# Kernel optimization log

Measured on AMD Instinct MI355X. Metric: run time of the kernel, lower is better.

Reference implementation:

```python
import math
import jax, jax.numpy as jnp
import numpy as np

B, S, E, H = 4, 2048, 1024, 16
HD = E // H  # 64


def setup_inputs() -> dict:
    key = jax.random.key(0)
    ks = jax.random.split(key, 7)
    scale = 1.0 / math.sqrt(E)
    return {
        "x": jax.random.normal(ks[0], (B, S, E), dtype=jnp.float32),
        "Wq": jax.random.normal(ks[1], (H, HD, E), dtype=jnp.float32) * scale,
        "bq": jax.random.normal(ks[2], (H, HD), dtype=jnp.float32) * 0.01,
        "Wk": jax.random.normal(ks[3], (H, HD, E), dtype=jnp.float32) * scale,
        "bk": jax.random.normal(ks[4], (H, HD), dtype=jnp.float32) * 0.01,
        "Wv": jax.random.normal(ks[5], (H, HD, E), dtype=jnp.float32) * scale,
        "bv": jax.random.normal(ks[6], (H, HD), dtype=jnp.float32) * 0.01,
    }


def reference(x, Wq, bq, Wk, bk, Wv, bv):
    b, s, e = x.shape
    h, hd, _ = Wq.shape
    inv_scale = 1.0 / math.sqrt(hd)
    # per-head linear projections (torch Linear: x @ W^T + b), batched over heads
    q = jnp.einsum("bse,hde->bshd", x, Wq) + bq  # [B,S,H,HD]
    k = jnp.einsum("bse,hde->bshd", x, Wk) + bk
    v = jnp.einsum("bse,hde->bshd", x, Wv) + bv
    # causal mask: -inf above diagonal (added before scaling, as in source;
    # -inf * inv_scale is still -inf so math is identical)
    mask = jnp.triu(jnp.full((s, s), -jnp.inf, dtype=x.dtype), k=1)
    scores = (jnp.einsum("bqhd,bkhd->bhqk", q, k) + mask) * inv_scale  # [B,H,S,S]
    attn = jax.nn.softmax(scores, axis=-1)
    out = jnp.einsum("bhqk,bkhd->bqhd", attn, v)  # [B,S,H,HD]
    # concat over heads in head order == reshape with head-major last dims
    return out.reshape(b, s, h * hd)
```

## Files before the change

### kernel.cpp

```cpp
#include <hip/hip_runtime.h>


typedef __bf16 bf16x8 __attribute__((ext_vector_type(8)));
typedef __bf16 bf16x4 __attribute__((ext_vector_type(4)));
typedef float f32x4 __attribute__((ext_vector_type(4)));
typedef unsigned short us8 __attribute__((ext_vector_type(8)));
typedef unsigned short us4 __attribute__((ext_vector_type(4)));

#define Bb 4
#define Ss 2048
#define Ee 1024
#define Hh 16
#define HD 64

#if __has_builtin(__builtin_amdgcn_exp2f)
#define EXP2(x) __builtin_amdgcn_exp2f(x)
#else
#define EXP2(x) exp2f(x)
#endif

__device__ __forceinline__ unsigned short f2bf(float f) {
  union { float f; unsigned u; } v; v.f = f;
  unsigned u = v.u;
  u += 0x7fffu + ((u >> 16) & 1u);
  return (unsigned short)(u >> 16);
}

__device__ __forceinline__ void gl_lds16(const void* g, void* l) {
  __builtin_amdgcn_global_load_lds((const __attribute__((address_space(1))) void*)g,
                                   (__attribute__((address_space(3))) void*)l, 16, 0, 0);
}

__global__ __launch_bounds__(256) void cvt_all(const float* __restrict__ x,
                                               const float* __restrict__ wq,
                                               const float* __restrict__ wk,
                                               const float* __restrict__ wv,
                                               unsigned short* __restrict__ xb,
                                               unsigned short* __restrict__ wb) {
  int i = blockIdx.x * 256 + threadIdx.x;
  const float* src; unsigned short* dst; int idx;
  if (i < 2097152)      { src = x;  dst = xb;                idx = i; }
  else if (i < 2359296) { src = wq; dst = wb;                idx = i - 2097152; }
  else if (i < 2621440) { src = wk; dst = wb + 1048576;      idx = i - 2359296; }
  else                  { src = wv; dst = wb + 2 * 1048576;  idx = i - 2621440; }
  float4 f = ((const float4*)src)[idx];
  us4 o = { f2bf(f.x), f2bf(f.y), f2bf(f.z), f2bf(f.w) };
  ((us4*)dst)[idx] = o;
}

__global__ __launch_bounds__(256) void qkv_gemm(const unsigned short* __restrict__ xb,
                                                const unsigned short* __restrict__ wb_all,
                                                const float* __restrict__ bq,
                                                const float* __restrict__ bk,
                                                const float* __restrict__ bv,
                                                unsigned short* __restrict__ qkv) {
  const int z = blockIdx.z;
  const unsigned short* wb = wb_all + (size_t)z * (Ee * Ee);
  const float* bias = (z == 0) ? bq : (z == 1) ? bk : bv;
  unsigned short* outb = qkv + (size_t)z * (Bb * Ss * Ee);
  const float osc = (z == 0) ? 0.180336880f : 1.0f;

  __shared__ unsigned short SMEM[16384];
  unsigned short* As = SMEM;
  unsigned short* Bs = SMEM + 8192;

  const int t = threadIdx.x;
  const int wave = t >> 6, lane = t & 63, quad = lane >> 4, ln = lane & 15;
  const int wm = wave & 1, wn = wave >> 1;
  const int m0 = blockIdx.x * 128, n0 = blockIdx.y * 128;

  const int srow = t >> 2;
  const int scol = (t & 3) * 8;

  f32x4 acc[4][4] = {};

  const unsigned short* ga = xb + (size_t)(m0 + srow) * Ee + scol;
  const unsigned short* gb = wb + (size_t)(n0 + srow) * Ee + scol;
  unsigned short* la = &As[t * 8];
  unsigned short* lb = &Bs[t * 8];

  for (int k0 = 0; k0 < Ee; k0 += 64) {
    __syncthreads();
    gl_lds16(ga + k0,                la);
    gl_lds16(ga + k0 + 64 * Ee,      la + 64 * 32);
    gl_lds16(gb + k0,                lb);
    gl_lds16(gb + k0 + 64 * Ee,      lb + 64 * 32);
    gl_lds16(ga + k0 + 32,           la + 4096);
    gl_lds16(ga + k0 + 32 + 64 * Ee, la + 4096 + 64 * 32);
    gl_lds16(gb + k0 + 32,           lb + 4096);
    gl_lds16(gb + k0 + 32 + 64 * Ee, lb + 4096 + 64 * 32);
    __syncthreads();
#pragma unroll
    for (int p = 0; p < 2; ++p) {
      bf16x8 af[4], bfr[4];
#pragma unroll
      for (int i = 0; i < 4; ++i)
        af[i] = *(const bf16x8*)&As[p * 4096 + (wm * 64 + i * 16 + ln) * 32 + quad * 8];
#pragma unroll
      for (int j = 0; j < 4; ++j)
        bfr[j] = *(const bf16x8*)&Bs[p * 4096 + (wn * 64 + j * 16 + ln) * 32 + quad * 8];
#pragma unroll
      for (int i = 0; i < 4; ++i)
#pragma unroll
        for (int j = 0; j < 4; ++j)
          acc[i][j] = __builtin_amdgcn_mfma_f32_16x16x32_bf16(af[i], bfr[j], acc[i][j], 0, 0, 0);
    }
  }

  float biasj[4];
#pragma unroll
  for (int j = 0; j < 4; ++j) biasj[j] = bias[n0 + wn * 64 + j * 16 + ln];

  if (z != 2) {
#pragma unroll
    for (int i = 0; i < 4; ++i)
#pragma unroll
      for (int j = 0; j < 4; ++j)
#pragma unroll
        for (int r = 0; r < 4; ++r) {
          int m = m0 + wm * 64 + i * 16 + quad * 4 + r;
          int n = n0 + wn * 64 + j * 16 + ln;
          int b_ = m >> 11, s = m & 2047;
          int h = n >> 6, d = n & 63;
          outb[(((size_t)b_ * Hh + h) * Ss + s) * HD + d] = f2bf((acc[i][j][r] + biasj[j]) * osc);
        }
  } else {
    for (int half = 0; half < 2; ++half) {
      __syncthreads();
      if (wm == half) {
#pragma unroll
        for (int i = 0; i < 4; ++i)
#pragma unroll
          for (int j = 0; j < 4; ++j)
#pragma unroll
            for (int r = 0; r < 4; ++r) {
              int mr = i * 16 + quad * 4 + r;
              int nc = wn * 64 + j * 16 + ln;
              SMEM[nc * 72 + mr] = f2bf(acc[i][j][r] + biasj[j]);
            }
      }
      __syncthreads();
      int nr = t >> 1;
      int n = n0 + nr;
      int h = n >> 6, d = n & 63;
      int mbase = m0 + half * 64 + (t & 1) * 32;
      int b_ = mbase >> 11;
#pragma unroll
      for (int q = 0; q < 4; ++q) {
        int s = (mbase & 2047) + q * 8;
        us8 vdat = *(const us8*)&SMEM[nr * 72 + (t & 1) * 32 + q * 8];
        *(us8*)&outb[(((size_t)b_ * Hh + h) * HD + d) * Ss + s] = vdat;
      }
    }
  }
}

__global__ __launch_bounds__(256) void flash_attn(const unsigned short* __restrict__ qkv,
                                                  float* __restrict__ out) {
  const int id = blockIdx.x;
  const int bh = id & 63;
  const int p = id >> 6;
  const int b_ = bh >> 4, h = bh & 15;

  const unsigned short* qb  = qkv + (size_t)bh * (Ss * HD);
  const unsigned short* kb  = qkv + (size_t)(64 + bh) * (Ss * HD);
  const unsigned short* vtb = qkv + (size_t)(128 + bh) * (Ss * HD);

  __shared__ __bf16 Ks[4096];
  __shared__ __bf16 Vt[4096];
  __shared__ __bf16 Ps[4][2][16][72];

  const int t = threadIdx.x;
  const int wave = t >> 6, lane = t & 63, quad = lane >> 4, ln = lane & 15;

  const int r0 = t >> 3;
  const int c0 = ((t & 7) ^ (r0 & 7)) * 8;
  const int koff0 = r0 * HD + c0;
  const int koff1 = koff0 + 32 * HD;
  const int voff0 = r0 * Ss + c0;
  const int voff1 = voff0 + 32 * Ss;
  __bf16* Kl0 = &Ks[t * 8];  __bf16* Kl1 = &Ks[2048 + t * 8];
  __bf16* Vl0 = &Vt[t * 8];  __bf16* Vl1 = &Vt[2048 + t * 8];

  int kslot[4][2];
#pragma unroll
  for (int g = 0; g < 4; ++g)
#pragma unroll
    for (int ks = 0; ks < 2; ++ks)
      kslot[g][ks] = ((g * 16 + ln) * 8 + ((ks * 4 + quad) ^ (ln & 7))) * 8;

  bf16x8 onef;
#pragma unroll
  for (int j = 0; j < 8; ++j) onef[j] = (__bf16)1.0f;

  const int qtps[2] = { 15 - p, p };

  for (int ph = 0; ph < 2; ++ph) {
    const int qtp = qtps[ph];
    const int q0 = qtp * 128;

    bf16x8 qf[2][2];
#pragma unroll
    for (int u = 0; u < 2; ++u)
#pragma unroll
      for (int ks = 0; ks < 2; ++ks)
        qf[u][ks] = *(const bf16x8*)(qb + (size_t)(q0 + u * 64 + wave * 16 + ln) * HD +
                                     ks * 32 + quad * 8);

    f32x4 o[2][4] = {};
    f32x4 l4[2] = {};
    const int ktmax = 2 * qtp + 1;

    for (int kt = 0; kt <= ktmax; ++kt) {
      const unsigned short* kbt = kb + kt * (64 * HD);
      const unsigned short* vbt = vtb + kt * 64;
      __syncthreads();
      gl_lds16(kbt + koff0, Kl0);
      gl_lds16(kbt + koff1, Kl1);
      gl_lds16(vbt + voff0, Vl0);
      gl_lds16(vbt + voff1, Vl1);
      __syncthreads();

#pragma unroll
      for (int u = 0; u < 2; ++u) {
        if (u == 0 && kt == ktmax) continue;
        const int qrow = q0 + u * 64 + wave * 16 + ln;

        f32x4 s_acc[4] = {};
#pragma unroll
        for (int g = 0; g < 4; ++g)
#pragma unroll
          for (int ks = 0; ks < 2; ++ks) {
            bf16x8 kf = *(const bf16x8*)&Ks[kslot[g][ks]];
            s_acc[g] = __builtin_amdgcn_mfma_f32_16x16x32_bf16(kf, qf[u][ks], s_acc[g], 0, 0, 0);
          }

        if (kt == 2 * qtp + u) {
          const int k0 = kt * 64;
#pragma unroll
          for (int g = 0; g < 4; ++g)
#pragma unroll
            for (int r = 0; r < 4; ++r) {
              int kcol = k0 + g * 16 + quad * 4 + r;
              if (kcol > qrow) s_acc[g][r] = -__builtin_inff();
            }
        }

#pragma unroll
        for (int g = 0; g < 4; ++g) {
          bf16x4 pk = { (__bf16)EXP2(s_acc[g][0]), (__bf16)EXP2(s_acc[g][1]),
                        (__bf16)EXP2(s_acc[g][2]), (__bf16)EXP2(s_acc[g][3]) };
          *(bf16x4*)&Ps[wave][u][ln][g * 16 + quad * 4] = pk;
        }
        bf16x8 pf[2];
#pragma unroll
        for (int ks = 0; ks < 2; ++ks)
          pf[ks] = *(const bf16x8*)&Ps[wave][u][ln][ks * 32 + quad * 8];

        l4[u] = __builtin_amdgcn_mfma_f32_16x16x32_bf16(pf[0], onef, l4[u], 0, 0, 0);
        l4[u] = __builtin_amdgcn_mfma_f32_16x16x32_bf16(pf[1], onef, l4[u], 0, 0, 0);

#pragma unroll
        for (int g = 0; g < 4; ++g)
#pragma unroll
          for (int ks = 0; ks < 2; ++ks) {
            bf16x8 vf = *(const bf16x8*)&Vt[kslot[g][ks]];
            o[u][g] = __builtin_amdgcn_mfma_f32_16x16x32_bf16(pf[ks], vf, o[u][g], 0, 0, 0);
          }
      }
    }

#pragma unroll
    for (int u = 0; u < 2; ++u) {
      float linv[4];
#pragma unroll
      for (int r = 0; r < 4; ++r) linv[r] = 1.0f / l4[u][r];
#pragma unroll
      for (int g = 0; g < 4; ++g)
#pragma unroll
        for (int r = 0; r < 4; ++r) {
          int orow = q0 + u * 64 + wave * 16 + quad * 4 + r;
          out[((size_t)b_ * Ss + orow) * Ee + h * HD + g * 16 + ln] = o[u][g][r] * linv[r];
        }
    }
    __syncthreads();
  }
}

extern "C" void kernel_launch(void* const* d_in, const int* in_sizes, int n_in,
                              void* d_out, int out_size, void* d_ws, size_t ws_size,
                              hipStream_t stream) {
  const float* x  = (const float*)d_in[0];
  const float* Wq = (const float*)d_in[1];
  const float* bq = (const float*)d_in[2];
  const float* Wk = (const float*)d_in[3];
  const float* bk = (const float*)d_in[4];
  const float* Wv = (const float*)d_in[5];
  const float* bv = (const float*)d_in[6];
  float* out = (float*)d_out;

  unsigned short* ws  = (unsigned short*)d_ws;
  unsigned short* xb  = ws;
  unsigned short* wb  = ws + 8388608;
  unsigned short* qkv = ws + 8388608 + 3 * 1048576;

  cvt_all<<<11264, 256, 0, stream>>>(x, Wq, Wk, Wv, xb, wb);
  qkv_gemm<<<dim3(64, 8, 3), 256, 0, stream>>>(xb, wb, bq, bk, bv, qkv);
  flash_attn<<<512, 256, 0, stream>>>(qkv, out);
}
```

Measured before the change: 219.9 us.

## Rewrite QKV GEMM with 256x256 tiles, double-buffered LDS and swizzled layout

The QKV projection GEMM moves from 128x128 tiles with 256 threads to 256x256 tiles with 512 threads. It double-buffers LDS across K steps, interleaving the next tile's global-to-LDS loads with MFMA quadrants, gated by explicit vmcnt waits, barriers and setprio. LDS is XOR-swizzled to avoid bank conflicts. The aim is to raise data reuse per block and hide global load latency. The cost is a 128 KB LDS footprint, only 384 blocks, and fragile hand-written synchronisation.

```diff
diff --git a/kernel.cpp b/kernel.cpp
--- a/kernel.cpp
+++ b/kernel.cpp
@@ -48,108 +48,235 @@
   ((us4*)dst)[idx] = o;
 }
 
-__global__ __launch_bounds__(256) void qkv_gemm(const unsigned short* __restrict__ xb,
-                                                const unsigned short* __restrict__ wb_all,
-                                                const float* __restrict__ bq,
-                                                const float* __restrict__ bk,
-                                                const float* __restrict__ bv,
-                                                unsigned short* __restrict__ qkv) {
+__global__ __launch_bounds__(512, 2) void qkv_gemm(const unsigned short* __restrict__ xb,
+                                                   const unsigned short* __restrict__ wb_all,
+                                                   const float* __restrict__ bq,
+                                                   const float* __restrict__ bk,
+                                                   const float* __restrict__ bv,
+                                                   unsigned short* __restrict__ qkv) {
   const int z = blockIdx.z;
   const unsigned short* wb = wb_all + (size_t)z * (Ee * Ee);
   const float* bias = (z == 0) ? bq : (z == 1) ? bk : bv;
   unsigned short* outb = qkv + (size_t)z * (Bb * Ss * Ee);
   const float osc = (z == 0) ? 0.180336880f : 1.0f;
 
-  __shared__ unsigned short SMEM[16384];
-  unsigned short* As = SMEM;
-  unsigned short* Bs = SMEM + 8192;
+  __shared__ unsigned short SMEM[65536];
 
   const int t = threadIdx.x;
   const int wave = t >> 6, lane = t & 63, quad = lane >> 4, ln = lane & 15;
-  const int wm = wave & 1, wn = wave >> 1;
-  const int m0 = blockIdx.x * 128, n0 = blockIdx.y * 128;
-
-  const int srow = t >> 2;
-  const int scol = (t & 3) * 8;
-
-  f32x4 acc[4][4] = {};
-
-  const unsigned short* ga = xb + (size_t)(m0 + srow) * Ee + scol;
-  const unsigned short* gb = wb + (size_t)(n0 + srow) * Ee + scol;
-  unsigned short* la = &As[t * 8];
-  unsigned short* lb = &Bs[t * 8];
-
-  for (int k0 = 0; k0 < Ee; k0 += 64) {
-    __syncthreads();
-    gl_lds16(ga + k0,                la);
-    gl_lds16(ga + k0 + 64 * Ee,      la + 64 * 32);
-    gl_lds16(gb + k0,                lb);
-    gl_lds16(gb + k0 + 64 * Ee,      lb + 64 * 32);
-    gl_lds16(ga + k0 + 32,           la + 4096);
-    gl_lds16(ga + k0 + 32 + 64 * Ee, la + 4096 + 64 * 32);
-    gl_lds16(gb + k0 + 32,           lb + 4096);
-    gl_lds16(gb + k0 + 32 + 64 * Ee, lb + 4096 + 64 * 32);
-    __syncthreads();
-#pragma unroll
-    for (int p = 0; p < 2; ++p) {
-      bf16x8 af[4], bfr[4];
-#pragma unroll
-      for (int i = 0; i < 4; ++i)
-        af[i] = *(const bf16x8*)&As[p * 4096 + (wm * 64 + i * 16 + ln) * 32 + quad * 8];
-#pragma unroll
-      for (int j = 0; j < 4; ++j)
-        bfr[j] = *(const bf16x8*)&Bs[p * 4096 + (wn * 64 + j * 16 + ln) * 32 + quad * 8];
-#pragma unroll
-      for (int i = 0; i < 4; ++i)
-#pragma unroll
-        for (int j = 0; j < 4; ++j)
-          acc[i][j] = __builtin_amdgcn_mfma_f32_16x16x32_bf16(af[i], bfr[j], acc[i][j], 0, 0, 0);
-    }
+  const int wr = wave >> 2, wc = wave & 3;
+  const int m0 = blockIdx.x * 256, n0 = blockIdx.y * 256;
+
+  const int r8 = t >> 3;
+  const int cs = ((t & 7) ^ (r8 & 7)) * 8;
+  const int t8 = t * 8;
+  const unsigned short* gA0 = xb + (size_t)(m0 + r8) * Ee + cs;
+  const unsigned short* gA1 = gA0 + 128 * Ee;
+  const unsigned short* gB0 = wb + (size_t)(n0 + r8) * Ee + cs;
+  const unsigned short* gB1 = gB0 + 128 * Ee;
+
+  int aoff0[4][2], boff0[2][2];
+#pragma unroll
+  for (int i = 0; i < 4; ++i)
+#pragma unroll
+    for (int kk = 0; kk < 2; ++kk)
+      aoff0[i][kk] = (wr * 64 + i * 16 + ln) * 64 + (((kk * 4 + quad) ^ (ln & 7)) * 8);
+#pragma unroll
+  for (int j = 0; j < 2; ++j)
+#pragma unroll
+    for (int kk = 0; kk < 2; ++kk)
+      boff0[j][kk] = 16384 + (wc * 32 + j * 16 + ln) * 64 + (((kk * 4 + quad) ^ (ln & 7)) * 8);
+
+  f32x4 acc[2][2][4][2] = {};
+
+  gl_lds16(gA0,           &SMEM[t8]);
+  gl_lds16(gA0 + 64 * Ee, &SMEM[t8 + 4096]);
+  gl_lds16(gB0,           &SMEM[16384 + t8]);
+  gl_lds16(gB0 + 64 * Ee, &SMEM[16384 + t8 + 4096]);
+  gl_lds16(gB1,           &SMEM[24576 + t8]);
+  gl_lds16(gB1 + 64 * Ee, &SMEM[24576 + t8 + 4096]);
+  gl_lds16(gA1,           &SMEM[8192 + t8]);
+  gl_lds16(gA1 + 64 * Ee, &SMEM[8192 + t8 + 4096]);
+
+#pragma unroll 1
+  for (int kt = 0; kt < 15; ++kt) {
+    const int cbuf = (kt & 1) << 15;
+    const int sbuf = cbuf ^ 32768;
+    const int co = (kt + 1) * 64;
+
+    bf16x8 af[4][2], bf0[2][2], bf1[2][2];
+
+    asm volatile("s_waitcnt vmcnt(4)" ::: "memory");
+    asm volatile("s_barrier" ::: "memory");
+#pragma unroll
+    for (int i = 0; i < 4; ++i)
+#pragma unroll
+      for (int kk = 0; kk < 2; ++kk)
+        af[i][kk] = *(const bf16x8*)&SMEM[cbuf + aoff0[i][kk]];
+#pragma unroll
+    for (int j = 0; j < 2; ++j)
+#pragma unroll
+      for (int kk = 0; kk < 2; ++kk)
+        bf0[j][kk] = *(const bf16x8*)&SMEM[cbuf + boff0[j][kk]];
+    gl_lds16(gA0 + co,           &SMEM[sbuf + t8]);
+    gl_lds16(gA0 + co + 64 * Ee, &SMEM[sbuf + t8 + 4096]);
+    asm volatile("s_barrier" ::: "memory");
+    __builtin_amdgcn_s_setprio(1);
+#pragma unroll
+    for (int i = 0; i < 4; ++i)
+#pragma unroll
+      for (int j = 0; j < 2; ++j)
+#pragma unroll
+        for (int kk = 0; kk < 2; ++kk)
+          acc[0][0][i][j] = __builtin_amdgcn_mfma_f32_16x16x32_bf16(af[i][kk], bf0[j][kk], acc[0][0][i][j], 0, 0, 0);
+    __builtin_amdgcn_s_setprio(0);
+
+    asm volatile("s_waitcnt vmcnt(4)" ::: "memory");
+    asm volatile("s_barrier" ::: "memory");
+#pragma unroll
+    for (int j = 0; j < 2; ++j)
+#pragma unroll
+      for (int kk = 0; kk < 2; ++kk)
+        bf1[j][kk] = *(const bf16x8*)&SMEM[cbuf + boff0[j][kk] + 8192];
+    gl_lds16(gB0 + co,           &SMEM[sbuf + 16384 + t8]);
+    gl_lds16(gB0 + co + 64 * Ee, &SMEM[sbuf + 16384 + t8 + 4096]);
+    asm volatile("s_barrier" ::: "memory");
+    __builtin_amdgcn_s_setprio(1);
+#pragma unroll
+    for (int i = 0; i < 4; ++i)
+#pragma unroll
+      for (int j = 0; j < 2; ++j)
+#pragma unroll
+        for (int kk = 0; kk < 2; ++kk)
+          acc[0][1][i][j] = __builtin_amdgcn_mfma_f32_16x16x32_bf16(af[i][kk], bf1[j][kk], acc[0][1][i][j], 0, 0, 0);
+    __builtin_amdgcn_s_setprio(0);
+
+    asm volatile("s_waitcnt vmcnt(4)" ::: "memory");
+    asm volatile("s_barrier" ::: "memory");
+#pragma unroll
+    for (int i = 0; i < 4; ++i)
+#pragma unroll
+      for (int kk = 0; kk < 2; ++kk)
+        af[i][kk] = *(const bf16x8*)&SMEM[cbuf + aoff0[i][kk] + 8192];
+    gl_lds16(gB1 + co,           &SMEM[sbuf + 24576 + t8]);
+    gl_lds16(gB1 + co + 64 * Ee, &SMEM[sbuf + 24576 + t8 + 4096]);
+    asm volatile("s_barrier" ::: "memory");
+    __builtin_amdgcn_s_setprio(1);
+#pragma unroll
+    for (int i = 0; i < 4; ++i)
+#pragma unroll
+      for (int j = 0; j < 2; ++j)
+#pragma unroll
+        for (int kk = 0; kk < 2; ++kk)
+          acc[1][0][i][j] = __builtin_amdgcn_mfma_f32_16x16x32_bf16(af[i][kk], bf0[j][kk], acc[1][0][i][j], 0, 0, 0);
+    __builtin_amdgcn_s_setprio(0);
+
+    asm volatile("s_barrier" ::: "memory");
+    gl_lds16(gA1 + co,           &SMEM[sbuf + 8192 + t8]);
+    gl_lds16(gA1 + co + 64 * Ee, &SMEM[sbuf + 8192 + t8 + 4096]);
+    asm volatile("s_barrier" ::: "memory");
+    __builtin_amdgcn_s_setprio(1);
+#pragma unroll
+    for (int i = 0; i < 4; ++i)
+#pragma unroll
+      for (int j = 0; j < 2; ++j)
+#pragma unroll
+        for (int kk = 0; kk < 2; ++kk)
+          acc[1][1][i][j] = __builtin_amdgcn_mfma_f32_16x16x32_bf16(af[i][kk], bf1[j][kk], acc[1][1][i][j], 0, 0, 0);
+    __builtin_amdgcn_s_setprio(0);
   }
 
-  float biasj[4];
-#pragma unroll
-  for (int j = 0; j < 4; ++j) biasj[j] = bias[n0 + wn * 64 + j * 16 + ln];
+  {
+    const int cbuf = 32768;
+    bf16x8 af[4][2], bf0[2][2], bf1[2][2];
+    asm volatile("s_waitcnt vmcnt(0)" ::: "memory");
+    asm volatile("s_barrier" ::: "memory");
+#pragma unroll
+    for (int i = 0; i < 4; ++i)
+#pragma unroll
+      for (int kk = 0; kk < 2; ++kk)
+        af[i][kk] = *(const bf16x8*)&SMEM[cbuf + aoff0[i][kk]];
+#pragma unroll
+    for (int j = 0; j < 2; ++j)
+#pragma unroll
+      for (int kk = 0; kk < 2; ++kk) {
+        bf0[j][kk] = *(const bf16x8*)&SMEM[cbuf + boff0[j][kk]];
+        bf1[j][kk] = *(const bf16x8*)&SMEM[cbuf + boff0[j][kk] + 8192];
+      }
+#pragma unroll
+    for (int i = 0; i < 4; ++i)
+#pragma unroll
+      for (int j = 0; j < 2; ++j)
+#pragma unroll
+        for (int kk = 0; kk < 2; ++kk) {
+          acc[0][0][i][j] = __builtin_amdgcn_mfma_f32_16x16x32_bf16(af[i][kk], bf0[j][kk], acc[0][0][i][j], 0, 0, 0);
+          acc[0][1][i][j] = __builtin_amdgcn_mfma_f32_16x16x32_bf16(af[i][kk], bf1[j][kk], acc[0][1][i][j], 0, 0, 0);
+        }
+#pragma unroll
+    for (int i = 0; i < 4; ++i)
+#pragma unroll
+      for (int kk = 0; kk < 2; ++kk)
+        af[i][kk] = *(const bf16x8*)&SMEM[cbuf + aoff0[i][kk] + 8192];
+#pragma unroll
+    for (int i = 0; i < 4; ++i)
+#pragma unroll
+      for (int j = 0; j < 2; ++j)
+#pragma unroll
+        for (int kk = 0; kk < 2; ++kk) {
+          acc[1][0][i][j] = __builtin_amdgcn_mfma_f32_16x16x32_bf16(af[i][kk], bf0[j][kk], acc[1][0][i][j], 0, 0, 0);
+          acc[1][1][i][j] = __builtin_amdgcn_mfma_f32_16x16x32_bf16(af[i][kk], bf1[j][kk], acc[1][1][i][j], 0, 0, 0);
+        }
+  }
+
+  float biasj[2][2];
+#pragma unroll
+  for (int qb = 0; qb < 2; ++qb)
+#pragma unroll
+    for (int j = 0; j < 2; ++j)
+      biasj[qb][j] = bias[n0 + qb * 128 + wc * 32 + j * 16 + ln];
 
   if (z != 2) {
 #pragma unroll
-    for (int i = 0; i < 4; ++i)
-#pragma unroll
-      for (int j = 0; j < 4; ++j)
-#pragma unroll
-        for (int r = 0; r < 4; ++r) {
-          int m = m0 + wm * 64 + i * 16 + quad * 4 + r;
-          int n = n0 + wn * 64 + j * 16 + ln;
-          int b_ = m >> 11, s = m & 2047;
-          int h = n >> 6, d = n & 63;
-          outb[(((size_t)b_ * Hh + h) * Ss + s) * HD + d] = f2bf((acc[i][j][r] + biasj[j]) * osc);
-        }
+    for (int qa = 0; qa < 2; ++qa)
+#pragma unroll
+      for (int qb = 0; qb < 2; ++qb)
+#pragma unroll
+        for (int i = 0; i < 4; ++i)
+#pragma unroll
+          for (int j = 0; j < 2; ++j)
+#pragma unroll
+            for (int r = 0; r < 4; ++r) {
+              int m = m0 + qa * 128 + wr * 64 + i * 16 + quad * 4 + r;
+              int n = n0 + qb * 128 + wc * 32 + j * 16 + ln;
+              int b_ = m >> 11, s = m & 2047;
+              int h = n >> 6, d = n & 63;
+              outb[(((size_t)b_ * Hh + h) * Ss + s) * HD + d] =
+                  f2bf((acc[qa][qb][i][j][r] + biasj[qb][j]) * osc);
+            }
   } else {
-    for (int half = 0; half < 2; ++half) {
+    for (int qa = 0; qa < 2; ++qa) {
       __syncthreads();
-      if (wm == half) {
+#pragma unroll
+      for (int qb = 0; qb < 2; ++qb)
 #pragma unroll
         for (int i = 0; i < 4; ++i)
 #pragma unroll
-          for (int j = 0; j < 4; ++j)
+          for (int j = 0; j < 2; ++j)
 #pragma unroll
             for (int r = 0; r < 4; ++r) {
-              int mr = i * 16 + quad * 4 + r;
-              int nc = wn * 64 + j * 16 + ln;
-              SMEM[nc * 72 + mr] = f2bf(acc[i][j][r] + biasj[j]);
+              int nc = qb * 128 + wc * 32 + j * 16 + ln;
+              int mr = wr * 64 + i * 16 + quad * 4 + r;
+              SMEM[nc * 136 + mr] = f2bf(acc[qa][qb][i][j][r] + biasj[qb][j]);
             }
-      }
       __syncthreads();
-      int nr = t >> 1;
-      int n = n0 + nr;
-      int h = n >> 6, d = n & 63;
-      int mbase = m0 + half * 64 + (t & 1) * 32;
-      int b_ = mbase >> 11;
-#pragma unroll
-      for (int q = 0; q < 4; ++q) {
-        int s = (mbase & 2047) + q * 8;
-        us8 vdat = *(const us8*)&SMEM[nr * 72 + (t & 1) * 32 + q * 8];
-        *(us8*)&outb[(((size_t)b_ * Hh + h) * HD + d) * Ss + s] = vdat;
+      int nr = t >> 1, mh = t & 1;
+      int n = n0 + nr, h = n >> 6, d = n & 63;
+      int b_ = m0 >> 11;
+      int s0 = (m0 & 2047) + qa * 128 + mh * 64;
+#pragma unroll
+      for (int q = 0; q < 8; ++q) {
+        us8 vdat = *(const us8*)&SMEM[nr * 136 + mh * 64 + q * 8];
+        *(us8*)&outb[(((size_t)b_ * Hh + h) * HD + d) * Ss + s0 + q * 8] = vdat;
       }
     }
   }
@@ -305,6 +432,6 @@
   unsigned short* qkv = ws + 8388608 + 3 * 1048576;
 
   cvt_all<<<11264, 256, 0, stream>>>(x, Wq, Wk, Wv, xb, wb);
-  qkv_gemm<<<dim3(64, 8, 3), 256, 0, stream>>>(xb, wb, bq, bk, bv, qkv);
+  qkv_gemm<<<dim3(32, 4, 3), 512, 0, stream>>>(xb, wb, bq, bk, bv, qkv);
   flash_attn<<<512, 256, 0, stream>>>(qkv, out);
 }
```

New measurement: 217.8 us. About the same (-1.0%).
